# Kernel tuning notes

Measured on AMD Instinct MI355X. Metric: run time of the kernel, lower is better.

## Reference

```python
import jax, jax.numpy as jnp
import numpy as np
from jax import lax

D_MODEL = 1024
D_FF = 4096
K = 5
PAD = K // 2


def setup_inputs() -> dict:
    key = jax.random.key(0)
    ks = jax.random.split(key, 12)
    s_in = 1.0 / np.sqrt(D_MODEL)
    s_ff = 1.0 / np.sqrt(D_FF)
    s_k = 1.0 / np.sqrt(K)  # depthwise conv fan_in = 1*K
    return {
        "x": jax.random.normal(ks[0], (4, 2048, D_MODEL), dtype=jnp.float32),
        "Wg": jax.random.uniform(ks[1], (D_MODEL, D_FF), jnp.float32, -s_in, s_in),
        "bg": jax.random.uniform(ks[2], (D_FF,), jnp.float32, -s_in, s_in),
        "Wu": jax.random.uniform(ks[3], (D_MODEL, D_FF), jnp.float32, -s_in, s_in),
        "bu": jax.random.uniform(ks[4], (D_FF,), jnp.float32, -s_in, s_in),
        "convg_w": jax.random.uniform(ks[5], (D_FF, 1, K), jnp.float32, -s_k, s_k),
        "convg_b": jax.random.uniform(ks[6], (D_FF,), jnp.float32, -s_k, s_k),
        "convu_w": jax.random.uniform(ks[7], (D_FF, 1, K), jnp.float32, -s_k, s_k),
        "convu_b": jax.random.uniform(ks[8], (D_FF,), jnp.float32, -s_k, s_k),
        "Wd": jax.random.uniform(ks[9], (D_FF, D_MODEL), jnp.float32, -s_ff, s_ff),
        "bd": jax.random.uniform(ks[10], (D_MODEL,), jnp.float32, -s_ff, s_ff),
    }


def _dwconv(h, w, b):
    # h: [B, L, C] -> depthwise conv along L with 'same' padding -> [B, L, C]
    y = lax.conv_general_dilated(
        h.transpose(0, 2, 1),  # [B, C, L]
        w,                      # [C, 1, K]
        window_strides=(1,),
        padding=[(PAD, PAD)],
        feature_group_count=h.shape[-1],
    )
    return (y + b[None, :, None]).transpose(0, 2, 1)


def reference(x, Wg, bg, Wu, bu, convg_w, convg_b, convu_w, convu_b, Wd, bd):
    gate = _dwconv(jnp.einsum("bld,df->blf", x, Wg) + bg, convg_w, convg_b)
    up = _dwconv(jnp.einsum("bld,df->blf", x, Wu) + bu, convu_w, convu_b)
    h = jax.nn.silu(gate) * up
    return jnp.einsum("blf,fd->bld", h, Wd) + bd
```

## Files before the change

### kernel.cpp

```cpp
#include <hip/hip_runtime.h>
#include <hip/hip_bf16.h>
#include <cstdint>

#define BATCH  4
#define SEQ    2048
#define DMODEL 1024
#define DFF    4096
#define MTOT   (BATCH * SEQ)
#define KCONV  5
#define PADC   2

using bf16raw = unsigned short;
typedef __attribute__((ext_vector_type(8))) short bf16x8;
typedef __attribute__((ext_vector_type(4))) float f32x4;

__device__ __forceinline__ float bf2f(bf16raw u) {
    return __uint_as_float(((uint32_t)u) << 16);
}
__device__ __forceinline__ bf16raw f2bf(float f) {
    uint32_t u = __float_as_uint(f);
    u = (u + 0x7fffu + ((u >> 16) & 1u)) >> 16;
    return (bf16raw)u;
}


__global__ __launch_bounds__(256)
void cvt_bf16_kernel(const float* __restrict__ in, bf16raw* __restrict__ out, int n4)
{
    const int i = blockIdx.x * 256 + threadIdx.x;
    if (i >= n4) return;
    const float4 v = reinterpret_cast<const float4*>(in)[i];
    ushort4 o;
    o.x = f2bf(v.x); o.y = f2bf(v.y); o.z = f2bf(v.z); o.w = f2bf(v.w);
    reinterpret_cast<ushort4*>(out)[i] = o;
}

__global__ __launch_bounds__(256)
void transpose_cvt_kernel(const float* __restrict__ in, bf16raw* __restrict__ out,
                          int R, int C)
{
    __shared__ float tile[32][33];
    const int r0 = blockIdx.y * 32, c0 = blockIdx.x * 32;
    const int tx = threadIdx.x & 31, ty = threadIdx.x >> 5;
#pragma unroll
    for (int i = 0; i < 4; ++i)
        tile[ty + i * 8][tx] = in[(size_t)(r0 + ty + i * 8) * C + c0 + tx];
    __syncthreads();
#pragma unroll
    for (int i = 0; i < 4; ++i)
        out[(size_t)(c0 + ty + i * 8) * R + r0 + tx] = f2bf(tile[tx][ty + i * 8]);
}

__global__ __launch_bounds__(256)
void convw_reorder_kernel(const float* __restrict__ wg, const float* __restrict__ wu,
                          float* __restrict__ wgT, float* __restrict__ wuT)
{
    const int i = blockIdx.x * 256 + threadIdx.x;
    if (i >= KCONV * DFF) return;
    const int j = i / DFF, f = i - j * DFF;
    wgT[i] = wg[f * KCONV + j];
    wuT[i] = wu[f * KCONV + j];
}


__device__ __forceinline__ void gll16(const bf16raw* g, const bf16raw* lds)
{
    __builtin_amdgcn_global_load_lds(
        (const __attribute__((address_space(1))) void*)g,
        (__attribute__((address_space(3))) void*)lds, 16, 0, 0);
}

template<typename CT, bool BIAS, int SPLITK>
__global__ __launch_bounds__(512, 2)
void gemm2b_kernel(const bf16raw* __restrict__ A, const bf16raw* __restrict__ BT,
                   const float* __restrict__ bias0, const float* __restrict__ bias1,
                   CT* __restrict__ C, int M, int N, int K, int nbm, int nbn)
{
    __shared__ bf16raw smem[2][2][256 * 32];

    const int tid  = threadIdx.x;
    const int lane = tid & 63;
    const int wave = __builtin_amdgcn_readfirstlane(tid >> 6);
    const int wr = wave >> 2;
    const int wc = wave & 3;

    const int nwg = nbm * nbn * SPLITK;
    const int cpx = nwg >> 3;
    const int bid = blockIdx.x;
    const int swz = (bid & 7) * cpx + (bid >> 3);
    int sk = 0, rem = swz;
    if constexpr (SPLITK > 1) { sk = swz / (nbm * nbn); rem = swz - sk * (nbm * nbn); }
    const int bx = rem / nbm;
    const int by = rem - bx * nbm;
    const int bm = by * 256;
    const int bn = bx * 256;

    const int klen = K / SPLITK;
    const int kbeg = sk * klen;
    const int NT   = klen / 32;
    CT* Cp = C + (size_t)sk * M * N;

    const int srow   = tid >> 2;
    const int schunk = tid & 3;

    auto stage = [&](int t, int buf) {
#pragma unroll
        for (int u = 0; u < 2; ++u) {
            const int ra = u * 128 + srow;
            gll16(A + (size_t)(bm + ra) * K + kbeg + t * 32
                    + ((schunk ^ ((ra >> 1) & 3)) << 3),
                  &smem[buf][0][ra * 32 + schunk * 8]);
        }
#pragma unroll
        for (int u = 0; u < 2; ++u) {
            const int rb = u * 128 + srow;
            gll16(BT + (size_t)(bn + rb) * K + kbeg + t * 32
                    + ((schunk ^ ((rb >> 1) & 3)) << 3),
                  &smem[buf][1][rb * 32 + schunk * 8]);
        }
    };

    const int g4  = lane >> 4;
    const int r15 = lane & 15;

    f32x4 acc[8][4];
#pragma unroll
    for (int i = 0; i < 8; ++i)
#pragma unroll
        for (int j = 0; j < 4; ++j) acc[i][j] = (f32x4){0.f, 0.f, 0.f, 0.f};

    auto compute = [&](int buf) {
        bf16x8 bfr[4];
#pragma unroll
        for (int nf = 0; nf < 4; ++nf) {
            const int row = wc * 64 + nf * 16 + r15;
            bfr[nf] = *(const bf16x8*)&smem[buf][1][row * 32 + ((g4 ^ ((row >> 1) & 3)) << 3)];
        }
        __builtin_amdgcn_s_setprio(1);
#pragma unroll
        for (int mf = 0; mf < 8; ++mf) {
            const int row = wr * 128 + mf * 16 + r15;
            const bf16x8 a = *(const bf16x8*)&smem[buf][0][row * 32 + ((g4 ^ ((row >> 1) & 3)) << 3)];
#pragma unroll
            for (int nf = 0; nf < 4; ++nf)
                acc[mf][nf] = __builtin_amdgcn_mfma_f32_16x16x32_bf16(
                    a, bfr[nf], acc[mf][nf], 0, 0, 0);
        }
        __builtin_amdgcn_s_setprio(0);
    };

    stage(0, 0);
    for (int t = 0; t < NT; ++t) {
        const int buf = t & 1;
        if (t + 1 < NT) {
            stage(t + 1, buf ^ 1);
            asm volatile("s_waitcnt vmcnt(4)" ::: "memory");
        } else {
            asm volatile("s_waitcnt vmcnt(0)" ::: "memory");
        }
        __builtin_amdgcn_s_barrier();
        compute(buf);
        __builtin_amdgcn_s_barrier();
    }

    const int er = g4 << 2;
#pragma unroll
    for (int nf = 0; nf < 4; ++nf) {
        const int nn = bn + wc * 64 + nf * 16 + r15;
        float bv = 0.f;
        if constexpr (BIAS) bv = (nn < DFF) ? bias0[nn] : bias1[nn - DFF];
#pragma unroll
        for (int mf = 0; mf < 8; ++mf) {
            const int mrow = bm + wr * 128 + mf * 16 + er;
#pragma unroll
            for (int j = 0; j < 4; ++j) {
                const float v = acc[mf][nf][j] + bv;
                if constexpr (sizeof(CT) == 2)
                    Cp[(size_t)(mrow + j) * N + nn] = f2bf(v);
                else
                    Cp[(size_t)(mrow + j) * N + nn] = v;
            }
        }
    }
}

template<int NS>
__global__ __launch_bounds__(256)
void reduce_bias_kernel(const float* __restrict__ part, const float* __restrict__ bd,
                        float* __restrict__ out)
{
    const int i = blockIdx.x * 256 + threadIdx.x;
    const int d = (i & (DMODEL / 4 - 1)) * 4;
    const float4 bb = *reinterpret_cast<const float4*>(bd + d);
    float4 o; o.x = bb.x; o.y = bb.y; o.z = bb.z; o.w = bb.w;
#pragma unroll
    for (int s = 0; s < NS; ++s) {
        const float4 a = reinterpret_cast<const float4*>(part + (size_t)s * MTOT * DMODEL)[i];
        o.x += a.x; o.y += a.y; o.z += a.z; o.w += a.w;
    }
    reinterpret_cast<float4*>(out)[i] = o;
}

__global__ __launch_bounds__(256)
void conv_silu_mul_bf16_kernel(const bf16raw* __restrict__ gp, const bf16raw* __restrict__ up,
                               const float* __restrict__ wgT, const float* __restrict__ cbg,
                               const float* __restrict__ wuT, const float* __restrict__ cbu,
                               bf16raw* __restrict__ h, int S)
{
    const int idx = blockIdx.x * 256 + threadIdx.x;
    const int f   = (idx & (DFF / 8 - 1)) << 3;
    const int row = idx >> 9;
    const int l   = row & (SEQ - 1);
    const int rb  = row - l;

    float g[8], u[8];
    {
        const float4 a0 = *reinterpret_cast<const float4*>(cbg + f);
        const float4 a1 = *reinterpret_cast<const float4*>(cbg + f + 4);
        const float4 b0 = *reinterpret_cast<const float4*>(cbu + f);
        const float4 b1 = *reinterpret_cast<const float4*>(cbu + f + 4);
        g[0]=a0.x; g[1]=a0.y; g[2]=a0.z; g[3]=a0.w; g[4]=a1.x; g[5]=a1.y; g[6]=a1.z; g[7]=a1.w;
        u[0]=b0.x; u[1]=b0.y; u[2]=b0.z; u[3]=b0.w; u[4]=b1.x; u[5]=b1.y; u[6]=b1.z; u[7]=b1.w;
    }

#pragma unroll
    for (int j = 0; j < KCONV; ++j) {
        const int ls = l + j - PADC;
        if (ls < 0 || ls >= SEQ) continue;
        const size_t off = (size_t)(rb + ls) * S + f;
        const bf16x8 gv = *reinterpret_cast<const bf16x8*>(gp + off);
        const bf16x8 uv = *reinterpret_cast<const bf16x8*>(up + off);
        const float4 wa0 = *reinterpret_cast<const float4*>(wgT + j * DFF + f);
        const float4 wa1 = *reinterpret_cast<const float4*>(wgT + j * DFF + f + 4);
        const float4 wb0 = *reinterpret_cast<const float4*>(wuT + j * DFF + f);
        const float4 wb1 = *reinterpret_cast<const float4*>(wuT + j * DFF + f + 4);
        const float wg8[8] = {wa0.x, wa0.y, wa0.z, wa0.w, wa1.x, wa1.y, wa1.z, wa1.w};
        const float wu8[8] = {wb0.x, wb0.y, wb0.z, wb0.w, wb1.x, wb1.y, wb1.z, wb1.w};
#pragma unroll
        for (int c = 0; c < 8; ++c) {
            g[c] += bf2f((bf16raw)gv[c]) * wg8[c];
            u[c] += bf2f((bf16raw)uv[c]) * wu8[c];
        }
    }

    bf16x8 hv;
#pragma unroll
    for (int c = 0; c < 8; ++c) {
        const float s = g[c] / (1.f + __expf(-g[c]));
        hv[c] = (short)f2bf(s * u[c]);
    }
    *reinterpret_cast<bf16x8*>(h + (size_t)row * DFF + f) = hv;
}


#define BM 128
#define BN 128
#define BK 8

__device__ __forceinline__ void load4f(const float* p, float v[4]) {
    const float4 t = *reinterpret_cast<const float4*>(p);
    v[0] = t.x; v[1] = t.y; v[2] = t.z; v[3] = t.w;
}

__global__ __launch_bounds__(256)
void sgemm_bias_kernel(const float* __restrict__ A, const float* __restrict__ B,
                       const float* __restrict__ bias, float* __restrict__ C,
                       int N, int K)
{
    __shared__ float As[BK][BM];
    __shared__ float Bs[BK][BN];

    const int tid = threadIdx.x;
    const int bm  = blockIdx.y * BM;
    const int bn  = blockIdx.x * BN;
    const int tx  = tid & 15;
    const int ty  = tid >> 4;

    const int arow = tid >> 1;
    const int acol = (tid & 1) * 4;
    const int brow = tid >> 5;
    const int bcol = (tid & 31) * 4;

    const float* Ap = A + (size_t)(bm + arow) * K + acol;
    const float* Bp = B + (size_t)brow * N + bn + bcol;

    float acc[8][8];
#pragma unroll
    for (int i = 0; i < 8; ++i)
#pragma unroll
        for (int j = 0; j < 8; ++j) acc[i][j] = 0.f;

    for (int k0 = 0; k0 < K; k0 += BK) {
        float av[4];
        load4f(Ap + k0, av);
        const float4 bv = *reinterpret_cast<const float4*>(Bp + (size_t)k0 * N);
        __syncthreads();
#pragma unroll
        for (int i = 0; i < 4; ++i) As[acol + i][arow] = av[i];
        *reinterpret_cast<float4*>(&Bs[brow][bcol]) = bv;
        __syncthreads();
#pragma unroll
        for (int kk = 0; kk < BK; ++kk) {
            const float4 a0 = *reinterpret_cast<const float4*>(&As[kk][ty * 4]);
            const float4 a1 = *reinterpret_cast<const float4*>(&As[kk][64 + ty * 4]);
            const float4 b0 = *reinterpret_cast<const float4*>(&Bs[kk][tx * 4]);
            const float4 b1 = *reinterpret_cast<const float4*>(&Bs[kk][64 + tx * 4]);
            const float am[8] = {a0.x, a0.y, a0.z, a0.w, a1.x, a1.y, a1.z, a1.w};
            const float bb[8] = {b0.x, b0.y, b0.z, b0.w, b1.x, b1.y, b1.z, b1.w};
#pragma unroll
            for (int mi = 0; mi < 8; ++mi)
#pragma unroll
                for (int nj = 0; nj < 8; ++nj)
                    acc[mi][nj] += am[mi] * bb[nj];
        }
    }
#pragma unroll
    for (int mi = 0; mi < 8; ++mi) {
        const int m = bm + ((mi < 4) ? (ty * 4 + mi) : (64 + ty * 4 + (mi - 4)));
#pragma unroll
        for (int g = 0; g < 2; ++g) {
            const int n = bn + g * 64 + tx * 4;
            float4 o;
            o.x = acc[mi][g * 4 + 0] + bias[n + 0];
            o.y = acc[mi][g * 4 + 1] + bias[n + 1];
            o.z = acc[mi][g * 4 + 2] + bias[n + 2];
            o.w = acc[mi][g * 4 + 3] + bias[n + 3];
            *reinterpret_cast<float4*>(&C[(size_t)m * N + n]) = o;
        }
    }
}

__global__ __launch_bounds__(256)
void conv_silu_mul_f32_kernel(const float* __restrict__ gp, const float* __restrict__ up,
                              const float* __restrict__ wg, const float* __restrict__ cbg,
                              const float* __restrict__ wu, const float* __restrict__ cbu,
                              float* __restrict__ hout)
{
    const int idx = blockIdx.x * 256 + threadIdx.x;
    const int f   = (idx & (DFF / 4 - 1)) * 4;
    const int l   = idx >> 10;

    float g[4], u[4];
    load4f(cbg + f, g);
    load4f(cbu + f, u);
#pragma unroll
    for (int j = 0; j < KCONV; ++j) {
        const int ls = l + j - PADC;
        if (ls < 0 || ls >= SEQ) continue;
        const size_t off = (size_t)ls * DFF + f;
        float gv[4], uv[4];
        load4f(gp + off, gv);
        load4f(up + off, uv);
#pragma unroll
        for (int c = 0; c < 4; ++c) {
            g[c] += gv[c] * wg[(f + c) * KCONV + j];
            u[c] += uv[c] * wu[(f + c) * KCONV + j];
        }
    }
    float h[4];
#pragma unroll
    for (int c = 0; c < 4; ++c) {
        const float s = g[c] / (1.f + __expf(-g[c]));
        h[c] = s * u[c];
    }
    float4 o; o.x = h[0]; o.y = h[1]; o.z = h[2]; o.w = h[3];
    *reinterpret_cast<float4*>(&hout[(size_t)l * DFF + f]) = o;
}


extern "C" void kernel_launch(void* const* d_in, const int* in_sizes, int n_in,
                              void* d_out, int out_size, void* d_ws, size_t ws_size,
                              hipStream_t stream)
{
    const float* x   = (const float*)d_in[0];
    const float* Wg  = (const float*)d_in[1];
    const float* bg  = (const float*)d_in[2];
    const float* Wu  = (const float*)d_in[3];
    const float* bu  = (const float*)d_in[4];
    const float* cgw = (const float*)d_in[5];
    const float* cgb = (const float*)d_in[6];
    const float* cuw = (const float*)d_in[7];
    const float* cub = (const float*)d_in[8];
    const float* Wd  = (const float*)d_in[9];
    const float* bd  = (const float*)d_in[10];
    float* out = (float*)d_out;

    const dim3 blk(256);
    auto align256 = [](size_t v) { return (v + 255) & ~(size_t)255; };

    const size_t SZ_XB  = (size_t)MTOT * DMODEL * 2;
    const size_t SZ_WGU = (size_t)2 * DFF * DMODEL * 2;
    const size_t SZ_WD  = (size_t)DMODEL * DFF * 2;
    const size_t SZ_CW  = (size_t)KCONV * DFF * 4;
    const size_t SZ_H   = (size_t)MTOT * DFF * 2;
    const size_t SZ_UP  = (size_t)MTOT * 2 * DFF * 2;

    size_t cur = 0;
    const size_t oXB  = cur; cur = align256(cur + SZ_XB);
    const size_t oWGU = cur; cur = align256(cur + SZ_WGU);
    const size_t oWD  = cur; cur = align256(cur + SZ_WD);
    const size_t oCWg = cur; cur = align256(cur + SZ_CW);
    const size_t oCWu = cur; cur = align256(cur + SZ_CW);
    const size_t oH   = cur; cur = align256(cur + SZ_H);
    const size_t oUP  = cur; cur = align256(cur + SZ_UP);
    const size_t need = cur;

    if (ws_size >= need) {
        bf16raw* xb   = (bf16raw*)((char*)d_ws + oXB);
        bf16raw* Wgu  = (bf16raw*)((char*)d_ws + oWGU);
        bf16raw* WdT  = (bf16raw*)((char*)d_ws + oWD);
        float*   cwg  = (float*)((char*)d_ws + oCWg);
        float*   cwu  = (float*)((char*)d_ws + oCWu);
        bf16raw* h    = (bf16raw*)((char*)d_ws + oH);
        bf16raw* Cup  = (bf16raw*)((char*)d_ws + oUP);
        float*   part = (float*)((char*)d_ws + oUP);

        cvt_bf16_kernel<<<(MTOT * DMODEL / 4 + 255) / 256, blk, 0, stream>>>(x, xb, MTOT * DMODEL / 4);
        transpose_cvt_kernel<<<dim3(DFF / 32, DMODEL / 32), blk, 0, stream>>>(Wg, Wgu, DMODEL, DFF);
        transpose_cvt_kernel<<<dim3(DFF / 32, DMODEL / 32), blk, 0, stream>>>(Wu, Wgu + (size_t)DFF * DMODEL, DMODEL, DFF);
        transpose_cvt_kernel<<<dim3(DMODEL / 32, DFF / 32), blk, 0, stream>>>(Wd, WdT, DFF, DMODEL);
        convw_reorder_kernel<<<(KCONV * DFF + 255) / 256, blk, 0, stream>>>(cgw, cuw, cwg, cwu);

        {
            const int nbm = MTOT / 256, nbn = (2 * DFF) / 256;
            gemm2b_kernel<bf16raw, true, 1><<<nbm * nbn, dim3(512), 0, stream>>>(
                xb, Wgu, bg, bu, Cup, MTOT, 2 * DFF, DMODEL, nbm, nbn);
        }

        conv_silu_mul_bf16_kernel<<<MTOT * (DFF / 8) / 256, blk, 0, stream>>>(
            Cup, Cup + DFF, cwg, cgb, cwu, cub, h, 2 * DFF);

        {
            const int nbm = MTOT / 256, nbn = DMODEL / 256;
            gemm2b_kernel<float, false, 4><<<nbm * nbn * 4, dim3(512), 0, stream>>>(
                h, WdT, nullptr, nullptr, part, MTOT, DMODEL, DFF, nbm, nbn);
        }
        reduce_bias_kernel<4><<<MTOT * DMODEL / 4 / 256, blk, 0, stream>>>(part, bd, out);
        return;
    }

    const size_t CE  = (size_t)SEQ * DFF;
    const size_t P32 = CE * sizeof(float);
    if (ws_size < 3 * P32) return;

    float* gpre = (float*)d_ws;
    float* upre = gpre + CE;
    float* hbuf = upre + CE;
    dim3 gu(DFF / BN, SEQ / BM);
    dim3 gdc(DMODEL / BN, SEQ / BM);
    const int nconv = SEQ * (DFF / 4) / 256;
    for (int b = 0; b < BATCH; ++b) {
        const float* xbp = x + (size_t)b * SEQ * DMODEL;
        float* outb = out + (size_t)b * SEQ * DMODEL;
        sgemm_bias_kernel<<<gu, blk, 0, stream>>>(xbp, Wg, bg, gpre, DFF, DMODEL);
        sgemm_bias_kernel<<<gu, blk, 0, stream>>>(xbp, Wu, bu, upre, DFF, DMODEL);
        conv_silu_mul_f32_kernel<<<nconv, blk, 0, stream>>>(gpre, upre, cgw, cgb, cuw, cub, hbuf);
        sgemm_bias_kernel<<<gdc, blk, 0, stream>>>(hbuf, Wd, bd, outb, DMODEL, DFF);
    }
}
```

Baseline: 432.3 us.

## Use 4-buffer LDS pipeline with prefetch distance two in bf16 GEMM

```diff
diff --git a/kernel.cpp b/kernel.cpp
--- a/kernel.cpp
+++ b/kernel.cpp
@@ -63,20 +63,20 @@
 }
 
 
-__device__ __forceinline__ void gll16(const bf16raw* g, const bf16raw* lds)
+__device__ __forceinline__ void gll16(const bf16raw* g, const char* lds)
 {
     __builtin_amdgcn_global_load_lds(
         (const __attribute__((address_space(1))) void*)g,
         (__attribute__((address_space(3))) void*)lds, 16, 0, 0);
 }
 
-template<typename CT, bool BIAS, int SPLITK>
+template<typename CT, bool BIAS, int SPLITK, bool COLMAJOR>
 __global__ __launch_bounds__(512, 2)
-void gemm2b_kernel(const bf16raw* __restrict__ A, const bf16raw* __restrict__ BT,
-                   const float* __restrict__ bias0, const float* __restrict__ bias1,
-                   CT* __restrict__ C, int M, int N, int K, int nbm, int nbn)
-{
-    __shared__ bf16raw smem[2][2][256 * 32];
+void gemmr_kernel(const bf16raw* __restrict__ A, const bf16raw* __restrict__ BT,
+                  const float* __restrict__ bias0, const float* __restrict__ bias1,
+                  CT* __restrict__ C, int M, int N, int K, int nbm, int nbn)
+{
+    __shared__ __align__(16) char smem[131072];
 
     const int tid  = threadIdx.x;
     const int lane = tid & 63;
@@ -90,8 +90,9 @@
     const int swz = (bid & 7) * cpx + (bid >> 3);
     int sk = 0, rem = swz;
     if constexpr (SPLITK > 1) { sk = swz / (nbm * nbn); rem = swz - sk * (nbm * nbn); }
-    const int bx = rem / nbm;
-    const int by = rem - bx * nbm;
+    int bx, by;
+    if constexpr (COLMAJOR) { bx = rem / nbm; by = rem - bx * nbm; }
+    else                    { by = rem / nbn; bx = rem - by * nbn; }
     const int bm = by * 256;
     const int bn = bx * 256;
 
@@ -100,67 +101,85 @@
     const int NT   = klen / 32;
     CT* Cp = C + (size_t)sk * M * N;
 
-    const int srow   = tid >> 2;
-    const int schunk = tid & 3;
-
-    auto stage = [&](int t, int buf) {
-#pragma unroll
-        for (int u = 0; u < 2; ++u) {
-            const int ra = u * 128 + srow;
-            gll16(A + (size_t)(bm + ra) * K + kbeg + t * 32
-                    + ((schunk ^ ((ra >> 1) & 3)) << 3),
-                  &smem[buf][0][ra * 32 + schunk * 8]);
-        }
-#pragma unroll
-        for (int u = 0; u < 2; ++u) {
-            const int rb = u * 128 + srow;
-            gll16(BT + (size_t)(bn + rb) * K + kbeg + t * 32
-                    + ((schunk ^ ((rb >> 1) & 3)) << 3),
-                  &smem[buf][1][rb * 32 + schunk * 8]);
-        }
+    const int srow  = tid >> 2;
+    const int sphys = tid & 3;
+
+    auto stageA = [&](int t, int half) {
+        const int row = half * 128 + srow;
+        gll16(A + (size_t)(bm + row) * K + kbeg + t * 32
+                + ((sphys ^ ((row >> 1) & 3)) << 3),
+              smem + (size_t)(t & 3) * 32768 + row * 64 + sphys * 16);
+    };
+    auto stageB = [&](int t, int half) {
+        const int row = half * 128 + srow;
+        gll16(BT + (size_t)(bn + row) * K + kbeg + t * 32
+                + ((sphys ^ ((row >> 1) & 3)) << 3),
+              smem + (size_t)(t & 3) * 32768 + 16384 + row * 64 + sphys * 16);
     };
 
     const int g4  = lane >> 4;
     const int r15 = lane & 15;
 
+    auto ldA = [&](int buf, int mf) -> bf16x8 {
+        const int row = wr * 128 + mf * 16 + r15;
+        return *(const bf16x8*)(smem + (size_t)buf * 32768 + row * 64
+                                + ((g4 ^ ((row >> 1) & 3)) << 4));
+    };
+    auto ldB = [&](int buf, int nf) -> bf16x8 {
+        const int row = wc * 64 + nf * 16 + r15;
+        return *(const bf16x8*)(smem + (size_t)buf * 32768 + 16384 + row * 64
+                                + ((g4 ^ ((row >> 1) & 3)) << 4));
+    };
+
     f32x4 acc[8][4];
 #pragma unroll
     for (int i = 0; i < 8; ++i)
 #pragma unroll
         for (int j = 0; j < 4; ++j) acc[i][j] = (f32x4){0.f, 0.f, 0.f, 0.f};
 
-    auto compute = [&](int buf) {
+    stageA(0, 0); stageA(0, 1); stageB(0, 0); stageB(0, 1);
+    stageA(1, 0); stageA(1, 1); stageB(1, 0); stageB(1, 1);
+
+    for (int t = 0; t < NT; ++t) {
+        const int buf = t & 3;
+        if (t < NT - 1) asm volatile("s_waitcnt vmcnt(4)" ::: "memory");
+        else            asm volatile("s_waitcnt vmcnt(0)" ::: "memory");
+        __builtin_amdgcn_s_barrier();
+        asm volatile("" ::: "memory");
+
+        if (t + 2 < NT) { stageA(t + 2, 0); stageA(t + 2, 1); }
         bf16x8 bfr[4];
 #pragma unroll
-        for (int nf = 0; nf < 4; ++nf) {
-            const int row = wc * 64 + nf * 16 + r15;
-            bfr[nf] = *(const bf16x8*)&smem[buf][1][row * 32 + ((g4 ^ ((row >> 1) & 3)) << 3)];
-        }
-        __builtin_amdgcn_s_setprio(1);
-#pragma unroll
-        for (int mf = 0; mf < 8; ++mf) {
-            const int row = wr * 128 + mf * 16 + r15;
-            const bf16x8 a = *(const bf16x8*)&smem[buf][0][row * 32 + ((g4 ^ ((row >> 1) & 3)) << 3)];
-#pragma unroll
-            for (int nf = 0; nf < 4; ++nf)
-                acc[mf][nf] = __builtin_amdgcn_mfma_f32_16x16x32_bf16(
-                    a, bfr[nf], acc[mf][nf], 0, 0, 0);
-        }
-        __builtin_amdgcn_s_setprio(0);
-    };
-
-    stage(0, 0);
-    for (int t = 0; t < NT; ++t) {
-        const int buf = t & 1;
-        if (t + 1 < NT) {
-            stage(t + 1, buf ^ 1);
-            asm volatile("s_waitcnt vmcnt(4)" ::: "memory");
-        } else {
-            asm volatile("s_waitcnt vmcnt(0)" ::: "memory");
-        }
-        __builtin_amdgcn_s_barrier();
-        compute(buf);
-        __builtin_amdgcn_s_barrier();
+        for (int nf = 0; nf < 4; ++nf) bfr[nf] = ldB(buf, nf);
+        {
+            bf16x8 afr[4];
+#pragma unroll
+            for (int i = 0; i < 4; ++i) afr[i] = ldA(buf, i);
+            __builtin_amdgcn_s_setprio(1);
+#pragma unroll
+            for (int i = 0; i < 4; ++i)
+#pragma unroll
+                for (int nf = 0; nf < 4; ++nf)
+                    acc[i][nf] = __builtin_amdgcn_mfma_f32_16x16x32_bf16(
+                        afr[i], bfr[nf], acc[i][nf], 0, 0, 0);
+            __builtin_amdgcn_s_setprio(0);
+        }
+
+        if (t + 2 < NT) { stageB(t + 2, 0); stageB(t + 2, 1); }
+        {
+            bf16x8 afr[4];
+#pragma unroll
+            for (int i = 0; i < 4; ++i) afr[i] = ldA(buf, 4 + i);
+            __builtin_amdgcn_s_setprio(1);
+#pragma unroll
+            for (int i = 0; i < 4; ++i)
+#pragma unroll
+                for (int nf = 0; nf < 4; ++nf)
+                    acc[4 + i][nf] = __builtin_amdgcn_mfma_f32_16x16x32_bf16(
+                        afr[i], bfr[nf], acc[4 + i][nf], 0, 0, 0);
+            __builtin_amdgcn_s_setprio(0);
+        }
+        asm volatile("" ::: "memory");
     }
 
     const int er = g4 << 2;
@@ -423,7 +442,7 @@
 
         {
             const int nbm = MTOT / 256, nbn = (2 * DFF) / 256;
-            gemm2b_kernel<bf16raw, true, 1><<<nbm * nbn, dim3(512), 0, stream>>>(
+            gemmr_kernel<bf16raw, true, 1, true><<<nbm * nbn, dim3(512), 0, stream>>>(
                 xb, Wgu, bg, bu, Cup, MTOT, 2 * DFF, DMODEL, nbm, nbn);
         }
 
@@ -432,10 +451,10 @@
 
         {
             const int nbm = MTOT / 256, nbn = DMODEL / 256;
-            gemm2b_kernel<float, false, 4><<<nbm * nbn * 4, dim3(512), 0, stream>>>(
+            gemmr_kernel<float, false, 2, false><<<nbm * nbn * 2, dim3(512), 0, stream>>>(
                 h, WdT, nullptr, nullptr, part, MTOT, DMODEL, DFF, nbm, nbn);
         }
-        reduce_bias_kernel<4><<<MTOT * DMODEL / 4 / 256, blk, 0, stream>>>(part, bd, out);
+        reduce_bias_kernel<2><<<MTOT * DMODEL / 4 / 256, blk, 0, stream>>>(part, bd, out);
         return;
     }
 
```

New measurement: 388.2 us. 10.2% less time.
